# Performance work log

Hardware: AMD Instinct MI355X
Metric: run time of the kernel (lower is better)

Reference implementation:

```python
import jax, jax.numpy as jnp
import numpy as np


def _gauss_kernel(scale):
    # se3cnn.util low_pass_filter: sigma = 0.5*sqrt(scale^2-1), size ~ 1+2*2.5*sigma (odd)
    sigma = 0.5 * float(np.sqrt(scale ** 2 - 1))
    size = int(1 + 2 * 2.5 * sigma)
    if size % 2 == 0:
        size += 1
    r = np.arange(size, dtype=np.float64) - size // 2
    g = np.exp(-r ** 2 / (2 * sigma ** 2))
    k3 = g[:, None, None] * g[None, :, None] * g[None, None, :]
    return (k3 / k3.sum()).astype(np.float32)

_K2 = jnp.asarray(_gauss_kernel(2))  # 5x5x5 Gaussian, scale=2
_DN = ('NCDHW', 'OIDHW', 'NCDHW')


def low_pass(x, stride):
    # depthwise Gaussian blur, padding = size//2 (=2)
    C = x.shape[1]
    k = jnp.tile(_K2[None, None], (C, 1, 1, 1, 1))  # [C,1,5,5,5]
    return jax.lax.conv_general_dilated(x, k, (stride,) * 3, [(2, 2)] * 3,
                                         dimension_numbers=_DN, feature_group_count=C)


def conv3d(x, w, pad):
    return jax.lax.conv_general_dilated(x, w, (1, 1, 1), [(pad, pad)] * 3,
                                         dimension_numbers=_DN)


def gated(x, n_scalar, caps):
    # caps: list of (multiplicity, 2l+1) for l>=1 capsules
    n_gate = sum(m for m, _ in caps)
    scal = jax.nn.relu(x[:, :n_scalar])
    if n_gate == 0:
        return scal
    gates = jax.nn.sigmoid(x[:, n_scalar:n_scalar + n_gate])
    parts = [scal]
    off = n_scalar + n_gate
    goff = 0
    B = x.shape[0]
    S = x.shape[2:]
    for m, d in caps:
        feat = x[:, off:off + m * d].reshape((B, m, d) + S)
        g = gates[:, goff:goff + m].reshape((B, m, 1) + S)
        parts.append((feat * g).reshape((B, m * d) + S))
        off += m * d
        goff += m
    return jnp.concatenate(parts, axis=1)


def gated_block(x, w, stride, n_scalar, caps):
    # smooth_stride: conv at stride 1, then strided low-pass (scale = stride)
    y = conv3d(x, w, pad=4)
    if stride > 1:
        y = low_pass(y, stride)
    return gated(y, n_scalar, caps)


def setup_inputs() -> dict:
    key = jax.random.key(0)
    ks = jax.random.split(key, 7)

    def w(k, shape):
        fan_in = int(np.prod(shape[1:]))
        return jax.random.normal(k, shape, jnp.float32) / np.sqrt(fan_in)

    return {
        'x': jax.random.normal(ks[0], (16, 1, 32, 32, 32), jnp.float32),
        'W1': w(ks[1], (30, 1, 5, 5, 5)),
        'W2': w(ks[2], (88, 25, 5, 5, 5)),
        'W3': w(ks[3], (96, 72, 5, 5, 5)),
        'W4': w(ks[4], (64, 80, 5, 5, 5)),
        'Wl': jax.random.normal(ks[5], (10, 64), jnp.float32) / 8.0,
        'bl': jnp.zeros((10,), jnp.float32),
    }


def reference(x, W1, W2, W3, W4, Wl, bl):
    h = low_pass(x, 1)                                   # input low-pass, scale=2
    h = gated_block(h, W1, 1, 2, [(2, 3), (2, 5), (1, 7)])   # -> 25 ch, 36^3
    h = gated_block(h, W2, 2, 8, [(8, 3), (8, 5)])           # -> 72 ch, 20^3
    h = gated_block(h, W3, 2, 16, [(8, 3), (8, 5)])          # -> 80 ch, 12^3
    h = gated_block(h, W4, 1, 64, [])                        # -> 64 ch, 16^3
    h = h.reshape(h.shape[0], h.shape[1], -1).mean(-1)       # AvgSpacial -> [B,64]
    # Dropout(p=0.2) is identity at eval time
    return h @ Wl.T + bl                                     # [B,10]
```

## Files before the change

### kernel.cpp

```cpp
#include <hip/hip_runtime.h>
#include <math.h>


struct GaussW { float g[5]; };
#define B_ 16

typedef __attribute__((ext_vector_type(8))) short bh8;
typedef __attribute__((ext_vector_type(16))) float f32v16;
union U128 { uint4 u; bh8 h; };

__device__ inline ushort f2bf(float f) {
  uint u = __float_as_uint(f);
  return (ushort)((u + 0x7FFFu + ((u >> 16) & 1u)) >> 16);
}

template<int NBC, int DZ, int DY, int DX, int AXIS, int EXP>
__global__ __launch_bounds__(256) void blur1d(
    const float* __restrict__ in, float* __restrict__ out, GaussW gw)
{
  constexpr int DZO = DZ + ((AXIS == 2 && EXP) ? 4 : 0);
  constexpr int DYO = DY + ((AXIS == 1 && EXP) ? 4 : 0);
  constexpr int OFF = EXP ? 4 : 2;
  constexpr int NV  = DX / 4;
  constexpr int TOT = NBC * DZO * DYO * NV;
  int idx = blockIdx.x * 256 + threadIdx.x;
  if (idx >= TOT) return;
  int xv = idx % NV;
  int t  = idx / NV;
  int y  = t % DYO;
  t /= DYO;
  int z  = t % DZO;
  int bc = t / DZO;
  const float* p = in + (size_t)bc * DZ * DY * DX;
  float4 s = make_float4(0.f, 0.f, 0.f, 0.f);
  #pragma unroll
  for (int k = 0; k < 5; ++k) {
    int c = (AXIS == 2 ? z : y) + k - OFF;
    if (c < 0 || c >= (AXIS == 2 ? DZ : DY)) continue;
    const float4 v = *(const float4*)(p +
        (AXIS == 2 ? ((size_t)c * DY + y) : ((size_t)z * DY + c)) * DX + 4 * xv);
    float g = gw.g[k];
    s.x = fmaf(g, v.x, s.x);
    s.y = fmaf(g, v.y, s.y);
    s.z = fmaf(g, v.z, s.z);
    s.w = fmaf(g, v.w, s.w);
  }
  *(float4*)(out + (((size_t)bc * DZO + z) * DYO + y) * DX + 4 * xv) = s;
}

template<int NBC, int DZ, int DY, int DXI>
__global__ __launch_bounds__(256) void blur1dx(
    const float* __restrict__ in, float* __restrict__ out, GaussW gw)
{
  constexpr int DXO = DXI + 4;
  static_assert(DXO % 4 == 0, "DXO must be /4");
  constexpr int NV  = DXO / 4;
  constexpr int TOT = NBC * DZ * DY * NV;
  int idx = blockIdx.x * 256 + threadIdx.x;
  if (idx >= TOT) return;
  int xv = idx % NV;
  int t  = idx / NV;
  int y  = t % DY;
  t /= DY;
  int z  = t % DZ;
  int bc = t / DZ;
  const float* row = in + ((size_t)bc * DZ + z) * DY * DXI + (size_t)y * DXI;
  float win[12];
  #pragma unroll
  for (int q = 0; q < 12; ++q) {
    int gx = 4 * xv + q - 4;
    win[q] = (gx >= 0 && gx < DXI) ? row[gx] : 0.f;
  }
  float o[4];
  #pragma unroll
  for (int q = 0; q < 4; ++q) {
    float s = 0.f;
    #pragma unroll
    for (int k = 0; k < 5; ++k) s = fmaf(gw.g[k], win[q + k], s);
    o[q] = s;
  }
  *(float4*)(out + (((size_t)bc * DZ + z) * DY + y) * DXO + 4 * xv) =
      make_float4(o[0], o[1], o[2], o[3]);
}

template<int CIN, int COUT, int COP>
__global__ __launch_bounds__(256) void k_transpose_w(
    const float* __restrict__ W, float* __restrict__ Wt)
{
  constexpr int TOT = CIN * 125 * COP;
  int idx = blockIdx.x * 256 + threadIdx.x;
  if (idx >= TOT) return;
  int co = idx % COP;
  int k  = (idx / COP) % 125;
  int ci = idx / (COP * 125);
  Wt[idx] = (co < COUT) ? W[((size_t)co * CIN + ci) * 125 + k] : 0.f;
}

template<int CIN, int NCHUNK, int COUT, int NCOT>
__global__ __launch_bounds__(256) void k_prep_w(
    const float* __restrict__ W, ushort* __restrict__ wf)
{
  constexpr int TOT = NCHUNK * 125 * NCOT * 2 * 512;
  int idx = blockIdx.x * 256 + threadIdx.x;
  if (idx >= TOT) return;
  int j    = idx & 7;
  int lane = (idx >> 3) & 63;
  int hl   = (idx >> 9) & 1;
  int t2   = idx >> 10;
  int cot  = t2 % NCOT;
  int kst  = t2 / NCOT;
  int tap  = kst % 125;
  int chunk = kst / 125;
  int ci = chunk * 16 + (lane >> 5) * 8 + j;
  int co = cot * 32 + (lane & 31);
  float w = 0.f;
  if (ci < CIN && co < COUT) w = W[((size_t)co * CIN + ci) * 125 + tap];
  ushort hi = f2bf(w);
  ushort v = hi;
  if (hl) { float hif = __uint_as_float((uint)hi << 16); v = f2bf(w - hif); }
  wf[idx] = v;
}

template<int S, int CIN, int NCHUNK, int COUT, int NCOT, int DIN, int XSRC,
         int DOUT, int PAD, int FUSEX, int XOFF>
__global__ __launch_bounds__(NCOT * 64)
void convM(const float* __restrict__ in, const ushort* __restrict__ wf,
           float* __restrict__ out, GaussW gw)
{
  constexpr int ZT = 2, YT = 4, XT = 4;
  constexpr int ZIN = (ZT - 1) * S + 5;
  constexpr int YIN = (YT - 1) * S + 5;
  constexpr int XIN = (XT - 1) * S + 5;
  constexpr int NPTS = ZIN * YIN * XIN;
  constexpr int RUS = 36;
  constexpr int NTH = NCOT * 64;
  constexpr int NXT = DOUT / XT, NYT = DOUT / YT, NZT = DOUT / ZT;
  static_assert(DOUT % XT == 0 && DOUT % YT == 0 && DOUT % ZT == 0, "tiles");
  constexpr int D2 = DOUT * DOUT;

  __shared__ __align__(16) uint s_in[NPTS * (RUS / 2)];
  ushort* s_us = (ushort*)s_in;

  const int tid  = threadIdx.x;
  const int lane = tid & 63;
  const int cot  = tid >> 6;
  int bxi = blockIdx.x;
  const int xt = bxi % NXT; bxi /= NXT;
  const int yt = bxi % NYT; bxi /= NYT;
  const int zt = bxi % NZT;
  const int b  = bxi / NZT;
  const int z0 = zt * ZT, y0 = yt * YT, x0 = xt * XT;

  const int n  = lane & 31, g = lane >> 5;
  const int zp = n >> 4, ny = (n >> 2) & 3, nx = n & 3;
  const int zl0 = S * zp, yl0 = S * ny, xl0 = S * nx;

  f32v16 ahh, ahl, alh;
  #pragma unroll
  for (int i = 0; i < 16; ++i) { ahh[i] = 0.f; ahl[i] = 0.f; alh[i] = 0.f; }

  #pragma unroll 1
  for (int chunk = 0; chunk < NCHUNK; ++chunk) {
    __syncthreads();
    #pragma unroll 1
    for (int e = tid; e < 16 * NPTS; e += NTH) {
      int cil = e / NPTS;
      int pt  = e - cil * NPTS;
      int sz = pt / (YIN * XIN);
      int r2 = pt - sz * (YIN * XIN);
      int sy = r2 / XIN;
      int sx = r2 - sy * XIN;
      int ci = chunk * 16 + cil;
      int gz = z0 * S + sz - PAD;
      int gy = y0 * S + sy - PAD;
      int gx = x0 * S + sx - PAD;
      float v = 0.f;
      if (ci < CIN && gz >= 0 && gz < DIN && gy >= 0 && gy < DIN) {
        const float* src = in +
            (((size_t)b * CIN + ci) * DIN + gz) * ((size_t)DIN * XSRC) +
            (size_t)gy * XSRC;
        if constexpr (FUSEX) {
          #pragma unroll
          for (int t = 0; t < 5; ++t) {
            int xs = gx - XOFF + t;
            if (xs >= 0 && xs < XSRC) v = fmaf(gw.g[t], src[xs], v);
          }
        } else {
          if (gx >= 0 && gx < XSRC) v = src[gx];
        }
      }
      ushort hi = f2bf(v);
      float hif = __uint_as_float((uint)hi << 16);
      ushort lo = f2bf(v - hif);
      s_us[pt * RUS + cil]      = hi;
      s_us[pt * RUS + 16 + cil] = lo;
    }
    __syncthreads();
    const ushort* wfc = wf + (size_t)chunk * 125 * NCOT * 2 * 512;
    #pragma unroll 1
    for (int kz = 0; kz < 5; ++kz) {
      #pragma unroll 1
      for (int ky = 0; ky < 5; ++ky) {
        const int rowb = ((zl0 + kz) * YIN + (yl0 + ky)) * XIN + xl0;
        for (int kx = 0; kx < 5; ++kx) {
          int tap = (kz * 5 + ky) * 5 + kx;
          const uint4* ap =
              (const uint4*)(wfc + (size_t)((tap * NCOT + cot) * 2) * 512);
          U128 wa, wl;
          wa.u = ap[lane];
          wl.u = ap[64 + lane];
          int pt = rowb + kx;
          const uint2* hp = (const uint2*)(s_us + pt * RUS + 8 * g);
          uint2 h0 = hp[0], h1 = hp[1];
          const uint2* lp = (const uint2*)(s_us + pt * RUS + 16 + 8 * g);
          uint2 l0 = lp[0], l1 = lp[1];
          U128 bh, bl;
          bh.u = make_uint4(h0.x, h0.y, h1.x, h1.y);
          bl.u = make_uint4(l0.x, l0.y, l1.x, l1.y);
          ahh = __builtin_amdgcn_mfma_f32_32x32x16_bf16(wa.h, bh.h, ahh, 0, 0, 0);
          ahl = __builtin_amdgcn_mfma_f32_32x32x16_bf16(wa.h, bl.h, ahl, 0, 0, 0);
          alh = __builtin_amdgcn_mfma_f32_32x32x16_bf16(wl.h, bh.h, alh, 0, 0, 0);
        }
      }
    }
  }
  #pragma unroll
  for (int r = 0; r < 16; ++r) {
    int co = cot * 32 + (r & 3) + 8 * (r >> 2) + 4 * g;
    if (co < COUT) {
      float s = ahh[r] + ahl[r] + alh[r];
      out[(((size_t)b * COUT + co) * DOUT + (z0 + zp)) * D2 +
          (size_t)(y0 + ny) * DOUT + (x0 + nx)] = s;
    }
  }
}

template<int S, int CIN, int CSPLIT, int COUT, int COP, int COB, int NCB,
         int DIN, int XSRC, int DOUT, int PAD, int ZT, int YT, int XB,
         int SPTP, int FUSEX, int XOFF, int CIB>
__global__ __launch_bounds__(256)
void convK(const float* __restrict__ in, const float* __restrict__ wt,
           float* __restrict__ out, size_t split_stride, GaussW gw)
{
  constexpr int K = 5;
  static_assert(DOUT % XB == 0, "XB must divide DOUT");
  constexpr int XQ  = DOUT / XB;
  constexpr int SPT = ZT * YT * XQ;
  static_assert(SPT <= SPTP, "SPTP too small");
  constexpr int NTH = SPTP * NCB;
  static_assert(NTH == 256, "block size 256");
  constexpr int XIN = (DOUT - 1) * S + K;
  constexpr int YIN = (YT - 1) * S + K;
  constexpr int ZIN = (ZT - 1) * S + K;
  constexpr int HXP = (S == 2) ? ((DOUT + 2 + 3) & ~3) : 0;
  constexpr int RW0 = (S == 2) ? (2 * HXP) : ((XIN + 3) & ~3);
  constexpr int RW  = (RW0 % 32 == 0 || RW0 % 32 == 16) ? (RW0 + 4) : RW0;
  constexpr int NROW = ZIN * YIN;
  constexpr int NIN  = NROW * RW;
  static_assert(DOUT % ZT == 0, "ZT must divide DOUT");
  constexpr int NZT = DOUT / ZT;
  constexpr int NYT = (DOUT + YT - 1) / YT;
  constexpr int D2  = DOUT * DOUT;
  constexpr int CI_PER = CIN / CSPLIT;
  static_assert(CI_PER % CIB == 0, "CIB must divide CI_PER");

  __shared__ __align__(16) float s_in[CIB][NIN];

  const int tid = threadIdx.x;
  const int cbg = __builtin_amdgcn_readfirstlane(tid / SPTP);
  const int sp  = tid % SPTP;

  const int bxi = blockIdx.x;
  const int yt  = bxi % NYT;
  const int zt  = (bxi / NYT) % NZT;
  const int b   = bxi / (NYT * NZT);
  const int cb  = blockIdx.y;
  const int spl = blockIdx.z;
  const int co0 = cb * (COB * NCB) + cbg * COB;
  const int oz0 = zt * ZT;
  const int oy0 = yt * YT;
  const int ci0 = spl * CI_PER;

  bool act = sp < SPT;
  int txq = act ? sp % XQ : 0;
  int t2  = act ? sp / XQ : 0;
  int tyl = t2 % YT;
  int tzl = t2 / YT;
  act = act && (oy0 + tyl < DOUT);
  if (!act) { txq = 0; tyl = 0; tzl = 0; }

  float acc[XB][COB];
  #pragma unroll
  for (int j = 0; j < XB; ++j)
    #pragma unroll
    for (int c = 0; c < COB; ++c) acc[j][c] = 0.f;

  for (int r = 0; r < CI_PER; r += CIB) {
    __syncthreads();
    for (int i = tid; i < CIB * NIN; i += NTH) {
      int cc = i / NIN;
      int w  = i - cc * NIN;
      int row = w / RW;
      int wx  = w - row * RW;
      int sz = row / YIN;
      int sy = row - sz * YIN;
      int u;
      if (S == 2) u = (wx < HXP) ? (2 * wx) : (wx < 2 * HXP ? 2 * (wx - HXP) + 1 : -1);
      else        u = (wx < XIN) ? wx : -1;
      int gz = oz0 * S + sz - PAD;
      int gy = oy0 * S + sy - PAD;
      int gx = u - PAD;
      float v = 0.f;
      if (u >= 0 && gz >= 0 && gz < DIN && gy >= 0 && gy < DIN &&
          gx >= 0 && gx < DIN) {
        const float* src = in +
            (((size_t)b * CIN + (ci0 + r + cc)) * DIN + gz) * ((size_t)DIN * XSRC) +
            (size_t)gy * XSRC;
        if constexpr (FUSEX) {
          float sacc = 0.f;
          #pragma unroll
          for (int tp = 0; tp < 5; ++tp) {
            int xs = gx + tp - XOFF;
            if (xs >= 0 && xs < XSRC) sacc = fmaf(gw.g[tp], src[xs], sacc);
          }
          v = sacc;
        } else {
          v = src[gx];
        }
      }
      s_in[cc][w] = v;
    }
    __syncthreads();
    #pragma unroll 1
    for (int cc = 0; cc < CIB; ++cc) {
      const int ci = ci0 + r + cc;
      const float* wci = wt + (size_t)ci * 125 * COP + co0;
      #pragma unroll 1
      for (int kz = 0; kz < K; ++kz) {
        #pragma unroll 1
        for (int ky = 0; ky < K; ++ky) {
          const float* rp = &s_in[cc][((tzl * S + kz) * YIN + (tyl * S + ky)) * RW];
          float fe[8], fo[8];
          if constexpr (S == 2) {
            const float* ep = rp + XB * txq;
            const float* op = rp + HXP + XB * txq;
            #pragma unroll
            for (int q = 0; q < 4; ++q) {
              float2 a = *(const float2*)(ep + 2 * q);
              fe[2*q] = a.x; fe[2*q+1] = a.y;
              float2 b2 = *(const float2*)(op + 2 * q);
              fo[2*q] = b2.x; fo[2*q+1] = b2.y;
            }
          } else {
            const float* wp0 = rp + XB * txq;
            float4 a = *(const float4*)wp0, b4 = *(const float4*)(wp0 + 4);
            fe[0]=a.x; fe[1]=a.y; fe[2]=a.z; fe[3]=a.w;
            fe[4]=b4.x; fe[5]=b4.y; fe[6]=b4.z; fe[7]=b4.w;
            fo[0]=0.f; fo[1]=0.f; fo[2]=0.f; fo[3]=0.f;
            fo[4]=0.f; fo[5]=0.f; fo[6]=0.f; fo[7]=0.f;
          }
          const float* wk = wci + (kz * 25 + ky * 5) * COP;
          #pragma unroll
          for (int kx = 0; kx < K; ++kx) {
            const float* wp = wk + kx * COP;
            float wv[COB];
            #pragma unroll
            for (int c = 0; c < COB; ++c) wv[c] = wp[c];
            #pragma unroll
            for (int j = 0; j < XB; ++j) {
              float iv;
              if constexpr (S == 2)
                iv = (kx & 1) ? fo[j + (kx >> 1)] : fe[j + (kx >> 1)];
              else
                iv = fe[j + kx];
              #pragma unroll
              for (int c = 0; c < COB; ++c)
                acc[j][c] = fmaf(iv, wv[c], acc[j][c]);
            }
          }
        }
      }
    }
  }
  if (act) {
    const int oz = oz0 + tzl, oy = oy0 + tyl, ox = txq * XB;
    float* ob = out + (size_t)spl * split_stride;
    #pragma unroll
    for (int c = 0; c < COB; ++c) {
      int co = co0 + c;
      if (co < COUT) {
        float* p = ob + (((size_t)b * COUT + co) * DOUT + oz) * D2 +
                   (size_t)oy * DOUT + ox;
        #pragma unroll
        for (int q = 0; q < XB / 2; ++q)
          *(float2*)(p + 2 * q) = make_float2(acc[2*q][c], acc[2*q+1][c]);
      }
    }
  }
}

__global__ __launch_bounds__(256) void k_gated4(
    const float* __restrict__ in, const float* __restrict__ in2,
    float* __restrict__ out, int S3v, int Cin, int n_scalar, int n_gate,
    int m1, int d1, int m2, int d2, int m3, int d3, int n_out)
{
  int idx = blockIdx.x * 256 + threadIdx.x;
  int oc = blockIdx.y;
  int b  = blockIdx.z;
  if (idx >= S3v) return;
  size_t S3 = (size_t)S3v * 4;
  auto ld = [&](int ch) {
    size_t o = ((size_t)b * Cin + ch) * S3 + 4 * (size_t)idx;
    float4 v = *(const float4*)(in + o);
    if (in2) {
      float4 w = *(const float4*)(in2 + o);
      v.x += w.x; v.y += w.y; v.z += w.z; v.w += w.w;
    }
    return v;
  };
  float4 val;
  if (oc < n_scalar) {
    float4 v = ld(oc);
    val = make_float4(fmaxf(v.x, 0.f), fmaxf(v.y, 0.f),
                      fmaxf(v.z, 0.f), fmaxf(v.w, 0.f));
  } else {
    int o = oc - n_scalar;
    int gate_ch;
    if (o < m1 * d1) gate_ch = n_scalar + o / d1;
    else if (o - m1 * d1 < m2 * d2) gate_ch = n_scalar + m1 + (o - m1 * d1) / d2;
    else gate_ch = n_scalar + m1 + m2 + (o - m1 * d1 - m2 * d2) / d3;
    float4 v = ld(n_scalar + n_gate + o);
    float4 g = ld(gate_ch);
    val = make_float4(v.x / (1.f + expf(-g.x)), v.y / (1.f + expf(-g.y)),
                      v.z / (1.f + expf(-g.z)), v.w / (1.f + expf(-g.w)));
  }
  *(float4*)(out + ((size_t)b * n_out + oc) * S3 + 4 * (size_t)idx) = val;
}

__global__ __launch_bounds__(256) void k_relu_avg(
    const float* __restrict__ in, float* __restrict__ h)
{
  int bc = blockIdx.x;
  const float* p = in + (size_t)bc * 4096;
  float s = 0.f;
  for (int i = threadIdx.x; i < 1024; i += 256) {
    float4 v = *(const float4*)(p + 4 * i);
    s += fmaxf(v.x, 0.f) + fmaxf(v.y, 0.f) + fmaxf(v.z, 0.f) + fmaxf(v.w, 0.f);
  }
  #pragma unroll
  for (int off = 32; off > 0; off >>= 1) s += __shfl_down(s, off, 64);
  __shared__ float wsum[4];
  int wid = threadIdx.x >> 6;
  if ((threadIdx.x & 63) == 0) wsum[wid] = s;
  __syncthreads();
  if (threadIdx.x == 0)
    h[bc] = (wsum[0] + wsum[1] + wsum[2] + wsum[3]) * (1.f / 4096.f);
}

__global__ __launch_bounds__(256) void k_linear(
    const float* __restrict__ h, const float* __restrict__ Wl,
    const float* __restrict__ bl, float* __restrict__ out)
{
  int t = threadIdx.x;
  if (t >= 160) return;
  int b = t / 10, o = t - b * 10;
  const float* hp = h + b * 64;
  const float* wp = Wl + o * 64;
  float s = bl[o];
  #pragma unroll
  for (int c = 0; c < 64; ++c) s = fmaf(hp[c], wp[c], s);
  out[t] = s;
}

extern "C" void kernel_launch(void* const* d_in, const int* in_sizes, int n_in,
                              void* d_out, int out_size, void* d_ws, size_t ws_size,
                              hipStream_t stream)
{
  const float* x  = (const float*)d_in[0];
  const float* W1 = (const float*)d_in[1];
  const float* W2 = (const float*)d_in[2];
  const float* W3 = (const float*)d_in[3];
  const float* W4 = (const float*)d_in[4];
  const float* Wl = (const float*)d_in[5];
  const float* bl = (const float*)d_in[6];
  float* out = (float*)d_out;
  float* ws  = (float*)d_ws;

  GaussW gw;
  {
    double gv[5], sum = 0.0;
    for (int i = 0; i < 5; ++i) { double r = i - 2; gv[i] = exp(-r * r / 1.5); sum += gv[i]; }
    for (int i = 0; i < 5; ++i) gw.g[i] = (float)(gv[i] / sum);
  }

  size_t off = 0;
  auto A = [&](size_t n) { size_t o = off; off += (n + 63) & ~(size_t)63; return o; };
  size_t o_lp  = A(524288);
  size_t o_W1t = A(4000);
  size_t o_Wf2 = A(384000);
  size_t o_Wf3 = A(960000);
  size_t o_Wf4 = A(640000);
  size_t o_h   = A(1024);
  size_t o_A   = A(23040000);
  size_t o_B   = A(22394880);
  if (ws_size < off * sizeof(float)) return;

  float*  lp  = ws + o_lp;
  float*  W1t = ws + o_W1t;
  ushort* Wf2 = (ushort*)(ws + o_Wf2);
  ushort* Wf3 = (ushort*)(ws + o_Wf3);
  ushort* Wf4 = (ushort*)(ws + o_Wf4);
  float*  hb  = ws + o_h;
  float*  Ab  = ws + o_A;
  float*  Bb  = ws + o_B;

  k_transpose_w<1, 30, 32><<<16, 256, 0, stream>>>(W1, W1t);
  k_prep_w<25, 2, 88, 3><<<(768000 + 255) / 256, 256, 0, stream>>>(W2, Wf2);
  k_prep_w<72, 5, 96, 3><<<(1920000 + 255) / 256, 256, 0, stream>>>(W3, Wf3);
  k_prep_w<80, 5, 64, 2><<<(1280000 + 255) / 256, 256, 0, stream>>>(W4, Wf4);

  blur1d<16, 32, 32, 32, 2, 0><<<(16 * 32 * 32 * 8 + 255) / 256, 256, 0, stream>>>(x, Ab, gw);
  blur1d<16, 32, 32, 32, 1, 0><<<(16 * 32 * 32 * 8 + 255) / 256, 256, 0, stream>>>(Ab, lp, gw);

  convK<1, 1, 1, 30, 32, 8, 2, 32, 32, 36, 4, 2, 7, 4, 128, 1, 2, 1>
      <<<dim3(16 * 18 * 6, 2, 1), 256, 0, stream>>>(lp, W1t, Bb, 0, gw);
  k_gated4<<<dim3(46, 25, 16), 256, 0, stream>>>(Bb, nullptr, Ab, 11664, 30, 2, 5,
                                                 2, 3, 2, 5, 1, 7, 25);
  blur1d<400, 36, 36, 36, 2, 1><<<(400 * 40 * 36 * 9 + 255) / 256, 256, 0, stream>>>(Ab, Bb, gw);
  blur1d<400, 40, 36, 36, 1, 1><<<(400 * 40 * 40 * 9 + 255) / 256, 256, 0, stream>>>(Bb, Ab, gw);
  convM<2, 25, 2, 88, 3, 40, 36, 20, 2, 1, 4>
      <<<dim3(16 * 10 * 5 * 5), 192, 0, stream>>>(Ab, Wf2, Bb, gw);
  k_gated4<<<dim3(8, 72, 16), 256, 0, stream>>>(Bb, nullptr, Ab, 2000, 88, 8, 16,
                                                8, 3, 8, 5, 0, 1, 72);
  blur1d<1152, 20, 20, 20, 2, 1><<<(1152 * 24 * 20 * 5 + 255) / 256, 256, 0, stream>>>(Ab, Bb, gw);
  blur1d<1152, 24, 20, 20, 1, 1><<<(1152 * 24 * 24 * 5 + 255) / 256, 256, 0, stream>>>(Bb, Ab, gw);
  blur1dx<1152, 24, 24, 20><<<(1152 * 24 * 24 * 6 + 255) / 256, 256, 0, stream>>>(Ab, Bb, gw);
  convM<2, 72, 5, 96, 3, 24, 24, 12, 2, 0, 0>
      <<<dim3(16 * 6 * 3 * 3), 192, 0, stream>>>(Bb, Wf3, Ab, gw);
  k_gated4<<<dim3(2, 80, 16), 256, 0, stream>>>(Ab, nullptr, Bb, 432, 96, 16, 16,
                                                8, 3, 8, 5, 0, 1, 80);
  convM<1, 80, 5, 64, 2, 12, 12, 16, 4, 0, 0>
      <<<dim3(16 * 8 * 4 * 4), 128, 0, stream>>>(Bb, Wf4, Ab, gw);
  k_relu_avg<<<1024, 256, 0, stream>>>(Ab, hb);
  k_linear<<<1, 256, 0, stream>>>(hb, Wl, bl, out);
}
```

Measured before the change: 2.643 ms.

## Pre-split activations into packed bf16 hi/lo pairs before convM staging

Measured after the change: 2.337 ms. 1.13x faster.

```diff
diff --git a/kernel.cpp b/kernel.cpp
--- a/kernel.cpp
+++ b/kernel.cpp
@@ -12,6 +12,12 @@
 __device__ inline ushort f2bf(float f) {
   uint u = __float_as_uint(f);
   return (ushort)((u + 0x7FFFu + ((u >> 16) & 1u)) >> 16);
+}
+__device__ inline uint packbf(float v) {
+  ushort hi = f2bf(v);
+  float hif = __uint_as_float((uint)hi << 16);
+  ushort lo = f2bf(v - hif);
+  return ((uint)hi << 16) | lo;
 }
 
 template<int NBC, int DZ, int DY, int DX, int AXIS, int EXP>
@@ -49,8 +55,8 @@
 }
 
 template<int NBC, int DZ, int DY, int DXI>
-__global__ __launch_bounds__(256) void blur1dx(
-    const float* __restrict__ in, float* __restrict__ out, GaussW gw)
+__global__ __launch_bounds__(256) void blur1dx_cvt(
+    const float* __restrict__ in, uint* __restrict__ out, GaussW gw)
 {
   constexpr int DXO = DXI + 4;
   static_assert(DXO % 4 == 0, "DXO must be /4");
@@ -71,16 +77,16 @@
     int gx = 4 * xv + q - 4;
     win[q] = (gx >= 0 && gx < DXI) ? row[gx] : 0.f;
   }
-  float o[4];
+  uint4 po;
+  uint* pp = (uint*)&po;
   #pragma unroll
   for (int q = 0; q < 4; ++q) {
     float s = 0.f;
     #pragma unroll
     for (int k = 0; k < 5; ++k) s = fmaf(gw.g[k], win[q + k], s);
-    o[q] = s;
-  }
-  *(float4*)(out + (((size_t)bc * DZ + z) * DY + y) * DXO + 4 * xv) =
-      make_float4(o[0], o[1], o[2], o[3]);
+    pp[q] = packbf(s);
+  }
+  *(uint4*)(out + (((size_t)bc * DZ + z) * DY + y) * DXO + 4 * xv) = po;
 }
 
 template<int CIN, int COUT, int COP>
@@ -121,11 +127,11 @@
   wf[idx] = v;
 }
 
-template<int S, int CIN, int NCHUNK, int COUT, int NCOT, int DIN, int XSRC,
-         int DOUT, int PAD, int FUSEX, int XOFF>
+template<int S, int CIN, int NCHUNK, int COUT, int NCOT, int DIN, int DOUT,
+         int PAD>
 __global__ __launch_bounds__(NCOT * 64)
-void convM(const float* __restrict__ in, const ushort* __restrict__ wf,
-           float* __restrict__ out, GaussW gw)
+void convM(const uint* __restrict__ in, const ushort* __restrict__ wf,
+           float* __restrict__ out)
 {
   constexpr int ZT = 2, YT = 4, XT = 4;
   constexpr int ZIN = (ZT - 1) * S + 5;
@@ -174,26 +180,13 @@
       int gz = z0 * S + sz - PAD;
       int gy = y0 * S + sy - PAD;
       int gx = x0 * S + sx - PAD;
-      float v = 0.f;
-      if (ci < CIN && gz >= 0 && gz < DIN && gy >= 0 && gy < DIN) {
-        const float* src = in +
-            (((size_t)b * CIN + ci) * DIN + gz) * ((size_t)DIN * XSRC) +
-            (size_t)gy * XSRC;
-        if constexpr (FUSEX) {
-          #pragma unroll
-          for (int t = 0; t < 5; ++t) {
-            int xs = gx - XOFF + t;
-            if (xs >= 0 && xs < XSRC) v = fmaf(gw.g[t], src[xs], v);
-          }
-        } else {
-          if (gx >= 0 && gx < XSRC) v = src[gx];
-        }
-      }
-      ushort hi = f2bf(v);
-      float hif = __uint_as_float((uint)hi << 16);
-      ushort lo = f2bf(v - hif);
-      s_us[pt * RUS + cil]      = hi;
-      s_us[pt * RUS + 16 + cil] = lo;
+      uint pk = 0;
+      if (ci < CIN && gz >= 0 && gz < DIN && gy >= 0 && gy < DIN &&
+          gx >= 0 && gx < DIN)
+        pk = in[((size_t)b * CIN + ci) * (DIN * DIN * DIN) +
+                (size_t)gz * (DIN * DIN) + gy * DIN + gx];
+      s_us[pt * RUS + cil]      = (ushort)(pk >> 16);
+      s_us[pt * RUS + 16 + cil] = (ushort)(pk & 0xFFFFu);
     }
     __syncthreads();
     const ushort* wfc = wf + (size_t)chunk * 125 * NCOT * 2 * 512;
@@ -400,8 +393,8 @@
 }
 
 __global__ __launch_bounds__(256) void k_gated4(
-    const float* __restrict__ in, const float* __restrict__ in2,
-    float* __restrict__ out, int S3v, int Cin, int n_scalar, int n_gate,
+    const float* __restrict__ in, float* __restrict__ out,
+    int S3v, int Cin, int n_scalar, int n_gate,
     int m1, int d1, int m2, int d2, int m3, int d3, int n_out)
 {
   int idx = blockIdx.x * 256 + threadIdx.x;
@@ -410,13 +403,7 @@
   if (idx >= S3v) return;
   size_t S3 = (size_t)S3v * 4;
   auto ld = [&](int ch) {
-    size_t o = ((size_t)b * Cin + ch) * S3 + 4 * (size_t)idx;
-    float4 v = *(const float4*)(in + o);
-    if (in2) {
-      float4 w = *(const float4*)(in2 + o);
-      v.x += w.x; v.y += w.y; v.z += w.z; v.w += w.w;
-    }
-    return v;
+    return *(const float4*)(in + ((size_t)b * Cin + ch) * S3 + 4 * (size_t)idx);
   };
   float4 val;
   if (oc < n_scalar) {
@@ -437,6 +424,39 @@
   *(float4*)(out + ((size_t)b * n_out + oc) * S3 + 4 * (size_t)idx) = val;
 }
 
+__global__ __launch_bounds__(256) void k_gated_pack(
+    const float* __restrict__ in, uint* __restrict__ out,
+    int S3v, int Cin, int n_scalar, int n_gate,
+    int m1, int d1, int m2, int d2, int n_out)
+{
+  int idx = blockIdx.x * 256 + threadIdx.x;
+  int oc = blockIdx.y;
+  int b  = blockIdx.z;
+  if (idx >= S3v) return;
+  size_t S3 = (size_t)S3v * 4;
+  auto ld = [&](int ch) {
+    return *(const float4*)(in + ((size_t)b * Cin + ch) * S3 + 4 * (size_t)idx);
+  };
+  float4 val;
+  if (oc < n_scalar) {
+    float4 v = ld(oc);
+    val = make_float4(fmaxf(v.x, 0.f), fmaxf(v.y, 0.f),
+                      fmaxf(v.z, 0.f), fmaxf(v.w, 0.f));
+  } else {
+    int o = oc - n_scalar;
+    int gate_ch;
+    if (o < m1 * d1) gate_ch = n_scalar + o / d1;
+    else gate_ch = n_scalar + m1 + (o - m1 * d1) / d2;
+    float4 v = ld(n_scalar + n_gate + o);
+    float4 g = ld(gate_ch);
+    val = make_float4(v.x / (1.f + expf(-g.x)), v.y / (1.f + expf(-g.y)),
+                      v.z / (1.f + expf(-g.z)), v.w / (1.f + expf(-g.w)));
+  }
+  uint4 po = make_uint4(packbf(val.x), packbf(val.y), packbf(val.z),
+                        packbf(val.w));
+  *(uint4*)(out + ((size_t)b * n_out + oc) * S3 + 4 * (size_t)idx) = po;
+}
+
 __global__ __launch_bounds__(256) void k_relu_avg(
     const float* __restrict__ in, float* __restrict__ h)
 {
@@ -502,7 +522,7 @@
   size_t o_Wf4 = A(640000);
   size_t o_h   = A(1024);
   size_t o_A   = A(23040000);
-  size_t o_B   = A(22394880);
+  size_t o_B   = A(25600000);
   if (ws_size < off * sizeof(float)) return;
 
   float*  lp  = ws + o_lp;
@@ -524,23 +544,26 @@
 
   convK<1, 1, 1, 30, 32, 8, 2, 32, 32, 36, 4, 2, 7, 4, 128, 1, 2, 1>
       <<<dim3(16 * 18 * 6, 2, 1), 256, 0, stream>>>(lp, W1t, Bb, 0, gw);
-  k_gated4<<<dim3(46, 25, 16), 256, 0, stream>>>(Bb, nullptr, Ab, 11664, 30, 2, 5,
+  k_gated4<<<dim3(46, 25, 16), 256, 0, stream>>>(Bb, Ab, 11664, 30, 2, 5,
                                                  2, 3, 2, 5, 1, 7, 25);
   blur1d<400, 36, 36, 36, 2, 1><<<(400 * 40 * 36 * 9 + 255) / 256, 256, 0, stream>>>(Ab, Bb, gw);
   blur1d<400, 40, 36, 36, 1, 1><<<(400 * 40 * 40 * 9 + 255) / 256, 256, 0, stream>>>(Bb, Ab, gw);
-  convM<2, 25, 2, 88, 3, 40, 36, 20, 2, 1, 4>
-      <<<dim3(16 * 10 * 5 * 5), 192, 0, stream>>>(Ab, Wf2, Bb, gw);
-  k_gated4<<<dim3(8, 72, 16), 256, 0, stream>>>(Bb, nullptr, Ab, 2000, 88, 8, 16,
+  blur1dx_cvt<400, 40, 40, 36><<<(400 * 40 * 40 * 10 + 255) / 256, 256, 0, stream>>>(
+      Ab, (uint*)Bb, gw);
+  convM<2, 25, 2, 88, 3, 40, 20, 2>
+      <<<dim3(16 * 10 * 5 * 5), 192, 0, stream>>>((const uint*)Bb, Wf2, Ab);
+  k_gated4<<<dim3(8, 72, 16), 256, 0, stream>>>(Ab, Bb, 2000, 88, 8, 16,
                                                 8, 3, 8, 5, 0, 1, 72);
-  blur1d<1152, 20, 20, 20, 2, 1><<<(1152 * 24 * 20 * 5 + 255) / 256, 256, 0, stream>>>(Ab, Bb, gw);
-  blur1d<1152, 24, 20, 20, 1, 1><<<(1152 * 24 * 24 * 5 + 255) / 256, 256, 0, stream>>>(Bb, Ab, gw);
-  blur1dx<1152, 24, 24, 20><<<(1152 * 24 * 24 * 6 + 255) / 256, 256, 0, stream>>>(Ab, Bb, gw);
-  convM<2, 72, 5, 96, 3, 24, 24, 12, 2, 0, 0>
-      <<<dim3(16 * 6 * 3 * 3), 192, 0, stream>>>(Bb, Wf3, Ab, gw);
-  k_gated4<<<dim3(2, 80, 16), 256, 0, stream>>>(Ab, nullptr, Bb, 432, 96, 16, 16,
-                                                8, 3, 8, 5, 0, 1, 80);
-  convM<1, 80, 5, 64, 2, 12, 12, 16, 4, 0, 0>
-      <<<dim3(16 * 8 * 4 * 4), 128, 0, stream>>>(Bb, Wf4, Ab, gw);
-  k_relu_avg<<<1024, 256, 0, stream>>>(Ab, hb);
+  blur1d<1152, 20, 20, 20, 2, 1><<<(1152 * 24 * 20 * 5 + 255) / 256, 256, 0, stream>>>(Bb, Ab, gw);
+  blur1d<1152, 24, 20, 20, 1, 1><<<(1152 * 24 * 24 * 5 + 255) / 256, 256, 0, stream>>>(Ab, Bb, gw);
+  blur1dx_cvt<1152, 24, 24, 20><<<(1152 * 24 * 24 * 6 + 255) / 256, 256, 0, stream>>>(
+      Bb, (uint*)Ab, gw);
+  convM<2, 72, 5, 96, 3, 24, 12, 2>
+      <<<dim3(16 * 6 * 3 * 3), 192, 0, stream>>>((const uint*)Ab, Wf3, Bb);
+  k_gated_pack<<<dim3(2, 80, 16), 256, 0, stream>>>(Bb, (uint*)Ab, 432, 96,
+                                                    16, 16, 8, 3, 8, 5, 80);
+  convM<1, 80, 5, 64, 2, 12, 16, 4>
+      <<<dim3(16 * 8 * 4 * 4), 128, 0, stream>>>((const uint*)Ab, Wf4, Bb);
+  k_relu_avg<<<1024, 256, 0, stream>>>(Bb, hb);
   k_linear<<<1, 256, 0, stream>>>(hb, Wl, bl, out);
 }
```
